# Optimization experiments

Hardware: AMD Instinct MI355X
Metric: run time of the kernel (lower is better)

Reference implementation:

```python
import jax, jax.numpy as jnp
import numpy as np

N = 50000   # nodes
E = 600000  # edges
D = 128     # in_feats = n_hidden
B = 16384   # pair batch
L = 2       # n_layers
C = 2       # n_classes
EPS = 1e-5


def setup_inputs() -> dict:
    key = jax.random.key(0)
    ks = jax.random.split(key, 16)
    s = 0.05
    return {
        "h": jax.random.normal(ks[0], (N, D), jnp.float32),
        "edge_src": jax.random.randint(ks[1], (E,), 0, N),
        "edge_dst": jax.random.randint(ks[2], (E,), 0, N),
        "x1": jax.random.randint(ks[3], (B,), 0, N),
        "x2": jax.random.randint(ks[4], (B,), 0, N),
        "x1_tar": jax.random.randint(ks[5], (B,), 0, N),
        "x2_tar": jax.random.randint(ks[6], (B,), 0, N),
        # SAGEConv params (mean aggregator): rst = h@W_self + mean_neigh@W_neigh + b
        "W_self": jax.random.normal(ks[7], (L, D, D), jnp.float32) * s,
        "W_neigh": jax.random.normal(ks[8], (L, D, D), jnp.float32) * s,
        "b_conv": jnp.zeros((L, D), jnp.float32),
        # head: linear1(3D->D) -> BN -> relu -> linear2(D->C)
        "W1": jax.random.normal(ks[9], (3 * D, D), jnp.float32) * s,
        "b1": jnp.zeros((D,), jnp.float32),
        "gamma": jnp.ones((D,), jnp.float32),
        "beta": jnp.zeros((D,), jnp.float32),
        "W2": jax.random.normal(ks[10], (D, C), jnp.float32) * s,
        "b2": jnp.zeros((C,), jnp.float32),
    }


def _sage_layers(h, edge_src, edge_dst, W_self, W_neigh, b_conv):
    # in-degree for mean aggregation (clamped to 1 to avoid div by 0)
    deg = jax.ops.segment_sum(jnp.ones((E,), h.dtype), edge_dst, num_segments=N)
    deg = jnp.maximum(deg, 1.0)[:, None]
    for l in range(L):
        msg = h[edge_src]                                        # [E, D] gather
        agg = jax.ops.segment_sum(msg, edge_dst, num_segments=N) / deg  # [N, D]
        h = jax.nn.relu(h @ W_self[l] + agg @ W_neigh[l] + b_conv[l])
    return h


def _pair_feat(h, a, b):
    ha, hb = h[a], h[b]
    return jnp.concatenate([ha, hb, jnp.abs(ha - hb)], axis=1)  # [B, 3D]


def _batchnorm(x, gamma, beta):
    m = x.mean(axis=0)
    v = x.var(axis=0)  # biased variance, as torch BN in training mode normalization
    return (x - m) * jax.lax.rsqrt(v + EPS) * gamma + beta


def reference(h, edge_src, edge_dst, x1, x2, x1_tar, x2_tar,
              W_self, W_neigh, b_conv, W1, b1, gamma, beta, W2, b2):
    h = _sage_layers(h, edge_src, edge_dst, W_self, W_neigh, b_conv)
    h_src = _pair_feat(h, x1, x2) @ W1 + b1
    h_tar = _pair_feat(h, x1_tar, x2_tar) @ W1 + b1
    h_src = _batchnorm(h_src, gamma, beta)
    h_tar = _batchnorm(h_tar, gamma, beta)
    h_src_mmd = jax.nn.relu(h_src)
    h_tar_mmd = jax.nn.relu(h_tar)
    h_p = h_src_mmd @ W2 + b2
    return (h_p, h_src_mmd, h_tar_mmd)
```

## Files before the change

kernel.cpp:

```cpp
#include <hip/hip_runtime.h>

#define NN 50000
#define NE 600000
#define DF 128
#define NB 16384
#define SCA_B 256
#define SCA_PER ((NE + SCA_B - 1) / SCA_B)
#define SCB_CAP 4352

typedef short bf16x8 __attribute__((ext_vector_type(8)));
typedef float f32x4 __attribute__((ext_vector_type(4)));

__device__ __forceinline__ float bf2f(unsigned short u){
  return __uint_as_float(((unsigned int)u) << 16);
}
__device__ __forceinline__ unsigned short f2bf(float x){
  unsigned int b = __float_as_uint(x);
  return (unsigned short)((b + 0x7FFFu + ((b >> 16) & 1u)) >> 16);
}

__global__ void GraphSAGE_8504035246140_kernel(){ }

__global__ __launch_bounds__(256) void k_prelude(
    const float* h_in, unsigned short* h_c,
    const float* Ws, const float* Wn, const float* W1,
    unsigned short* WsB, unsigned short* WnB, unsigned short* W1B,
    int* cnt, float* stats){
  int b = blockIdx.x, t = threadIdx.x;
  if (b < 3125){
    int i = b * 256 + t;
    const float4* s = (const float4*)h_in;
    float4 v0 = s[i * 2], v1 = s[i * 2 + 1];
    unsigned short d[8] = {f2bf(v0.x), f2bf(v0.y), f2bf(v0.z), f2bf(v0.w),
                           f2bf(v1.x), f2bf(v1.y), f2bf(v1.z), f2bf(v1.w)};
    *(bf16x8*)(h_c + i * 8) = *(bf16x8*)d;
  } else if (b < 3516){
    int i = (b - 3125) * 256 + t;
    if (i < 2 * NN) cnt[i] = 0;
  } else if (b < 3518){
    int i = (b - 3516) * 256 + t;
    if (i < 512) stats[i] = 0.f;
  } else {
    int idx = (b - 3518) * 256 + t;
    if (idx < 2 * DF * DF){
      int layer = idx >> 14;
      int e = idx & (DF * DF - 1);
      int k = e >> 7, n = e & 127;
      int dst = layer * DF * DF + (((k >> 3) * 128 + n) << 3) + (k & 7);
      WsB[dst] = f2bf(Ws[idx]);
      WnB[dst] = f2bf(Wn[idx]);
    }
    if (idx < 3 * DF * DF){
      int k = idx >> 7, n = idx & 127;
      W1B[(((k >> 3) * 128 + n) << 3) + (k & 7)] = f2bf(W1[idx]);
    }
  }
}

__global__ void k_hist(const int* dst, int* cnt){
  int e = blockIdx.x * 256 + threadIdx.x;
  if (e < NE) atomicAdd(&cnt[dst[e]], 1);
}
__global__ void k_scan1(const int* cnt, int* bsum){
  __shared__ int l[256];
  int t = threadIdx.x, i = blockIdx.x * 256 + t;
  l[t] = (i < NN) ? cnt[i] : 0;
  __syncthreads();
  for (int o = 128; o > 0; o >>= 1){
    if (t < o) l[t] += l[t + o];
    __syncthreads();
  }
  if (t == 0) bsum[blockIdx.x] = l[0];
}
__global__ void k_scan3(const int* cnt, const int* bsum, int* rp, int* cfill){
  __shared__ int bs[256];
  __shared__ int l[256];
  int t = threadIdx.x, i = blockIdx.x * 256 + t;
  bs[t] = (t < 196) ? bsum[t] : 0;
  int v = (i < NN) ? cnt[i] : 0;
  l[t] = v;
  __syncthreads();
  for (int o = 1; o < 256; o <<= 1){
    int xb = (t >= o) ? bs[t - o] : 0;
    int xl = (t >= o) ? l[t - o] : 0;
    __syncthreads();
    bs[t] += xb; l[t] += xl;
    __syncthreads();
  }
  int base = (blockIdx.x == 0) ? 0 : bs[blockIdx.x - 1];
  if (i < NN){
    int r = base + l[t] - v;
    rp[i] = r;
    if (t == 0) cfill[blockIdx.x] = r;
    if (i == NN - 1) rp[NN] = base + l[t];
  }
}

__global__ __launch_bounds__(256) void k_scatA(
    const int* src, const int* dst, int* cfill, unsigned int* tmp){
  __shared__ unsigned int hist[196];
  __shared__ unsigned int cursor[196];
  int t = threadIdx.x;
  int e0 = blockIdx.x * SCA_PER;
  int e1 = e0 + SCA_PER; if (e1 > NE) e1 = NE;
  if (t < 196) hist[t] = 0;
  __syncthreads();
  for (int e = e0 + t; e < e1; e += 256) atomicAdd(&hist[dst[e] >> 8], 1u);
  __syncthreads();
  if (t < 196) cursor[t] = (unsigned int)atomicAdd(&cfill[t], (int)hist[t]);
  __syncthreads();
  for (int e = e0 + t; e < e1; e += 256){
    int d = dst[e];
    unsigned int off = atomicAdd(&cursor[d >> 8], 1u);
    tmp[off] = (unsigned int)src[e] | ((unsigned int)(d & 255) << 16);
  }
}

__global__ __launch_bounds__(256) void k_scatB(
    const unsigned int* tmp, const int* rp, int* fill, int* perm){
  __shared__ unsigned int hist[256];
  __shared__ unsigned int sc[256];
  __shared__ unsigned int ebuf[SCB_CAP];
  __shared__ unsigned int sbuf[SCB_CAP];
  int b = blockIdx.x, t = threadIdx.x;
  int n0 = b << 8;
  int n1 = n0 + 256; if (n1 > NN) n1 = NN;
  int s = rp[n0], e = rp[n1];
  int cntb = e - s;
  if (cntb <= SCB_CAP){
    hist[t] = 0;
    __syncthreads();
    for (int i = t; i < cntb; i += 256){
      unsigned int v = tmp[s + i];
      ebuf[i] = v;
      atomicAdd(&hist[(v >> 16) & 255], 1u);
    }
    __syncthreads();
    unsigned int cntk = hist[t];
    sc[t] = cntk;
    __syncthreads();
    for (int o = 1; o < 256; o <<= 1){
      unsigned int x = (t >= o) ? sc[t - o] : 0;
      __syncthreads();
      sc[t] += x;
      __syncthreads();
    }
    hist[t] = sc[t] - cntk;
    __syncthreads();
    for (int i = t; i < cntb; i += 256){
      unsigned int v = ebuf[i];
      unsigned int off = atomicAdd(&hist[(v >> 16) & 255], 1u);
      sbuf[off] = v;
    }
    __syncthreads();
    for (int i = t; i < cntb; i += 256) perm[s + i] = (int)(sbuf[i] & 0xFFFFu);
  } else {
    for (int i = t; i < cntb; i += 256){
      unsigned int v = tmp[s + i];
      int node = n0 + (int)((v >> 16) & 255);
      int pos = atomicAdd(&fill[node], 1);
      perm[rp[node] + pos] = (int)(v & 0xFFFFu);
    }
  }
}

__global__ __launch_bounds__(256) void k_agg(
    const unsigned int* hb32, const int* rp, const int* perm,
    unsigned int* agg32){
  int n = blockIdx.x * 4 + (threadIdx.x >> 6);
  if (n >= NN) return;
  int l = threadIdx.x & 63;
  int rs = l >> 4, li = l & 15;
  int s = rp[n], e = rp[n + 1];
  const unsigned int* hq = hb32 + li * 4;
  float a0 = 0.f, a1 = 0.f, a2 = 0.f, a3 = 0.f;
  float a4 = 0.f, a5 = 0.f, a6 = 0.f, a7 = 0.f;
  int i = s;
  for (; i + 16 <= e; i += 16){
    int p0 = perm[i + rs];
    int p1 = perm[i + 4 + rs];
    int p2 = perm[i + 8 + rs];
    int p3 = perm[i + 12 + rs];
    uint4 x0 = *(const uint4*)(hq + (size_t)p0 * 64);
    uint4 x1 = *(const uint4*)(hq + (size_t)p1 * 64);
    uint4 x2 = *(const uint4*)(hq + (size_t)p2 * 64);
    uint4 x3 = *(const uint4*)(hq + (size_t)p3 * 64);
    a0 += __uint_as_float(x0.x << 16); a1 += __uint_as_float(x0.x & 0xffff0000u);
    a2 += __uint_as_float(x0.y << 16); a3 += __uint_as_float(x0.y & 0xffff0000u);
    a4 += __uint_as_float(x0.z << 16); a5 += __uint_as_float(x0.z & 0xffff0000u);
    a6 += __uint_as_float(x0.w << 16); a7 += __uint_as_float(x0.w & 0xffff0000u);
    a0 += __uint_as_float(x1.x << 16); a1 += __uint_as_float(x1.x & 0xffff0000u);
    a2 += __uint_as_float(x1.y << 16); a3 += __uint_as_float(x1.y & 0xffff0000u);
    a4 += __uint_as_float(x1.z << 16); a5 += __uint_as_float(x1.z & 0xffff0000u);
    a6 += __uint_as_float(x1.w << 16); a7 += __uint_as_float(x1.w & 0xffff0000u);
    a0 += __uint_as_float(x2.x << 16); a1 += __uint_as_float(x2.x & 0xffff0000u);
    a2 += __uint_as_float(x2.y << 16); a3 += __uint_as_float(x2.y & 0xffff0000u);
    a4 += __uint_as_float(x2.z << 16); a5 += __uint_as_float(x2.z & 0xffff0000u);
    a6 += __uint_as_float(x2.w << 16); a7 += __uint_as_float(x2.w & 0xffff0000u);
    a0 += __uint_as_float(x3.x << 16); a1 += __uint_as_float(x3.x & 0xffff0000u);
    a2 += __uint_as_float(x3.y << 16); a3 += __uint_as_float(x3.y & 0xffff0000u);
    a4 += __uint_as_float(x3.z << 16); a5 += __uint_as_float(x3.z & 0xffff0000u);
    a6 += __uint_as_float(x3.w << 16); a7 += __uint_as_float(x3.w & 0xffff0000u);
  }
  if (i < e){
    int i0 = i + rs, i1 = i + 4 + rs, i2 = i + 8 + rs, i3 = i + 12 + rs;
    int p0 = perm[i0 < e ? i0 : s];
    int p1 = perm[i1 < e ? i1 : s];
    int p2 = perm[i2 < e ? i2 : s];
    int p3 = perm[i3 < e ? i3 : s];
    uint4 x0 = *(const uint4*)(hq + (size_t)p0 * 64);
    uint4 x1 = *(const uint4*)(hq + (size_t)p1 * 64);
    uint4 x2 = *(const uint4*)(hq + (size_t)p2 * 64);
    uint4 x3 = *(const uint4*)(hq + (size_t)p3 * 64);
    if (i0 < e){
      a0 += __uint_as_float(x0.x << 16); a1 += __uint_as_float(x0.x & 0xffff0000u);
      a2 += __uint_as_float(x0.y << 16); a3 += __uint_as_float(x0.y & 0xffff0000u);
      a4 += __uint_as_float(x0.z << 16); a5 += __uint_as_float(x0.z & 0xffff0000u);
      a6 += __uint_as_float(x0.w << 16); a7 += __uint_as_float(x0.w & 0xffff0000u);
    }
    if (i1 < e){
      a0 += __uint_as_float(x1.x << 16); a1 += __uint_as_float(x1.x & 0xffff0000u);
      a2 += __uint_as_float(x1.y << 16); a3 += __uint_as_float(x1.y & 0xffff0000u);
      a4 += __uint_as_float(x1.z << 16); a5 += __uint_as_float(x1.z & 0xffff0000u);
      a6 += __uint_as_float(x1.w << 16); a7 += __uint_as_float(x1.w & 0xffff0000u);
    }
    if (i2 < e){
      a0 += __uint_as_float(x2.x << 16); a1 += __uint_as_float(x2.x & 0xffff0000u);
      a2 += __uint_as_float(x2.y << 16); a3 += __uint_as_float(x2.y & 0xffff0000u);
      a4 += __uint_as_float(x2.z << 16); a5 += __uint_as_float(x2.z & 0xffff0000u);
      a6 += __uint_as_float(x2.w << 16); a7 += __uint_as_float(x2.w & 0xffff0000u);
    }
    if (i3 < e){
      a0 += __uint_as_float(x3.x << 16); a1 += __uint_as_float(x3.x & 0xffff0000u);
      a2 += __uint_as_float(x3.y << 16); a3 += __uint_as_float(x3.y & 0xffff0000u);
      a4 += __uint_as_float(x3.z << 16); a5 += __uint_as_float(x3.z & 0xffff0000u);
      a6 += __uint_as_float(x3.w << 16); a7 += __uint_as_float(x3.w & 0xffff0000u);
    }
  }
  a0 += __shfl_xor(a0, 16); a1 += __shfl_xor(a1, 16);
  a2 += __shfl_xor(a2, 16); a3 += __shfl_xor(a3, 16);
  a4 += __shfl_xor(a4, 16); a5 += __shfl_xor(a5, 16);
  a6 += __shfl_xor(a6, 16); a7 += __shfl_xor(a7, 16);
  a0 += __shfl_xor(a0, 32); a1 += __shfl_xor(a1, 32);
  a2 += __shfl_xor(a2, 32); a3 += __shfl_xor(a3, 32);
  a4 += __shfl_xor(a4, 32); a5 += __shfl_xor(a5, 32);
  a6 += __shfl_xor(a6, 32); a7 += __shfl_xor(a7, 32);
  if (rs == 0){
    float di = 1.0f / fmaxf((float)(e - s), 1.0f);
    uint4 r;
    r.x = (unsigned int)f2bf(a0 * di) | ((unsigned int)f2bf(a1 * di) << 16);
    r.y = (unsigned int)f2bf(a2 * di) | ((unsigned int)f2bf(a3 * di) << 16);
    r.z = (unsigned int)f2bf(a4 * di) | ((unsigned int)f2bf(a5 * di) << 16);
    r.w = (unsigned int)f2bf(a6 * di) | ((unsigned int)f2bf(a7 * di) << 16);
    *(uint4*)(agg32 + (size_t)n * 64 + li * 4) = r;
  }
}

__global__ __launch_bounds__(256) void k_layer_mfma(
    const unsigned short* hb, const unsigned short* aggb,
    const unsigned short* WsB, const unsigned short* WnB,
    const float* bias, unsigned short* hout){
  int t = threadIdx.x;
  int w = t >> 6, l = t & 63;
  int m = l & 15, q = l >> 4;
  int r0 = blockIdx.x * 128 + w * 16;
  int arow0 = r0 + m;       if (arow0 > NN - 1) arow0 = NN - 1;
  int arow1 = r0 + 64 + m;  if (arow1 > NN - 1) arow1 = NN - 1;
  const unsigned short* hp0 = hb   + (size_t)arow0 * DF + q * 8;
  const unsigned short* ap0 = aggb + (size_t)arow0 * DF + q * 8;
  const unsigned short* hp1 = hb   + (size_t)arow1 * DF + q * 8;
  const unsigned short* ap1 = aggb + (size_t)arow1 * DF + q * 8;
  f32x4 acc0[8], acc1[8];
  for (int ct = 0; ct < 8; ++ct){
    float bbc = bias[ct * 16 + m];
    acc0[ct] = (f32x4){bbc, bbc, bbc, bbc};
    acc1[ct] = (f32x4){bbc, bbc, bbc, bbc};
  }
  for (int kt = 0; kt < 4; ++kt){
    bf16x8 a_h0 = *(const bf16x8*)(hp0 + kt * 32);
    bf16x8 a_g0 = *(const bf16x8*)(ap0 + kt * 32);
    bf16x8 a_h1 = *(const bf16x8*)(hp1 + kt * 32);
    bf16x8 a_g1 = *(const bf16x8*)(ap1 + kt * 32);
    int kg = kt * 4 + q;
    for (int ct = 0; ct < 8; ++ct){
      bf16x8 b_s = *(const bf16x8*)(WsB + (((kg << 7) + ct * 16 + m) << 3));
      bf16x8 b_n = *(const bf16x8*)(WnB + (((kg << 7) + ct * 16 + m) << 3));
      acc0[ct] = __builtin_amdgcn_mfma_f32_16x16x32_bf16(a_h0, b_s, acc0[ct], 0, 0, 0);
      acc0[ct] = __builtin_amdgcn_mfma_f32_16x16x32_bf16(a_g0, b_n, acc0[ct], 0, 0, 0);
      acc1[ct] = __builtin_amdgcn_mfma_f32_16x16x32_bf16(a_h1, b_s, acc1[ct], 0, 0, 0);
      acc1[ct] = __builtin_amdgcn_mfma_f32_16x16x32_bf16(a_g1, b_n, acc1[ct], 0, 0, 0);
    }
  }
  for (int ct = 0; ct < 8; ++ct){
    int col = ct * 16 + m;
    for (int reg = 0; reg < 4; ++reg){
      int row0 = r0 + q * 4 + reg;
      int row1 = row0 + 64;
      if (row0 < NN) hout[(size_t)row0 * DF + col] = f2bf(fmaxf(acc0[ct][reg], 0.f));
      if (row1 < NN) hout[(size_t)row1 * DF + col] = f2bf(fmaxf(acc1[ct][reg], 0.f));
    }
  }
}

__global__ __launch_bounds__(256) void k_pair_mfma(
    const unsigned short* h2,
    const int* x1, const int* x2, const int* x1t, const int* x2t,
    const unsigned short* W1B, const float* b1, float* zbase, float* stats){
  __shared__ __align__(16) unsigned short F[64 * 392];
  __shared__ float csum[128], csq[128];
  int g = blockIdx.y;
  const int* ia = g ? x1t : x1;
  const int* ib = g ? x2t : x2;
  float* z = zbase + (size_t)g * NB * DF;
  int t = threadIdx.x;
  if (t < 128){ csum[t] = 0.f; csq[t] = 0.f; }
  int r0 = blockIdx.x * 64;
  int i = t >> 2, qq = t & 3;
  int r = r0 + i;
  int a = ia[r], b = ib[r];
  const unsigned short* pa = h2 + (size_t)a * DF + qq * 32;
  const unsigned short* pb = h2 + (size_t)b * DF + qq * 32;
  unsigned short* fr = F + i * 392;
  for (int jj = 0; jj < 4; ++jj){
    bf16x8 va = *(const bf16x8*)(pa + jj * 8);
    bf16x8 vb = *(const bf16x8*)(pb + jj * 8);
    *(bf16x8*)(fr + qq * 32 + jj * 8) = va;
    *(bf16x8*)(fr + 128 + qq * 32 + jj * 8) = vb;
    unsigned short d[8];
    for (int e = 0; e < 8; ++e){
      float fa = bf2f((unsigned short)va[e]);
      float fb = bf2f((unsigned short)vb[e]);
      d[e] = f2bf(fabsf(fa - fb));
    }
    *(bf16x8*)(fr + 256 + qq * 32 + jj * 8) = *(bf16x8*)d;
  }
  __syncthreads();
  int w = t >> 6, l = t & 63;
  int m = l & 15, q = l >> 4;
  int rl = w * 16 + m;
  f32x4 acc[8];
  for (int ct = 0; ct < 8; ++ct){
    float bbc = b1[ct * 16 + m];
    acc[ct] = (f32x4){bbc, bbc, bbc, bbc};
  }
  for (int kt = 0; kt < 12; ++kt){
    bf16x8 af = *(const bf16x8*)(F + rl * 392 + kt * 32 + q * 8);
    int kg = kt * 4 + q;
    for (int ct = 0; ct < 8; ++ct){
      bf16x8 bfr = *(const bf16x8*)(W1B + (((kg << 7) + ct * 16 + m) << 3));
      acc[ct] = __builtin_amdgcn_mfma_f32_16x16x32_bf16(af, bfr, acc[ct], 0, 0, 0);
    }
  }
  for (int ct = 0; ct < 8; ++ct){
    int col = ct * 16 + m;
    int row = r0 + w * 16 + q * 4;
    float s = 0.f, s2 = 0.f;
    for (int reg = 0; reg < 4; ++reg){
      float v = acc[ct][reg];
      z[(size_t)(row + reg) * DF + col] = v;
      s += v; s2 += v * v;
    }
    atomicAdd(&csum[col], s);
    atomicAdd(&csq[col], s2);
  }
  __syncthreads();
  if (t < 128){
    atomicAdd(&stats[g * 256 + t], csum[t]);
    atomicAdd(&stats[g * 256 + 128 + t], csq[t]);
  }
}

__global__ __launch_bounds__(256) void k_norm_hp(
    const float* zbase, const float* stats,
    const float* gamma, const float* beta,
    const float* W2, const float* b2, float* mmd_base, float* hp){
  int g = blockIdx.y;
  int t = threadIdx.x;
  int w = t >> 6, l = t & 63;
  int c0 = l * 2, c1 = c0 + 1;
  float m0 = stats[g * 256 + c0] * (1.0f / NB);
  float m1 = stats[g * 256 + c1] * (1.0f / NB);
  float v0 = stats[g * 256 + 128 + c0] * (1.0f / NB) - m0 * m0;
  float v1 = stats[g * 256 + 128 + c1] * (1.0f / NB) - m1 * m1;
  float is0 = 1.0f / sqrtf(v0 + 1e-5f);
  float is1 = 1.0f / sqrtf(v1 + 1e-5f);
  float ga0 = gamma[c0], ga1 = gamma[c1];
  float be0 = beta[c0], be1 = beta[c1];
  float w200 = W2[c0 * 2], w201 = W2[c0 * 2 + 1];
  float w210 = W2[c1 * 2], w211 = W2[c1 * 2 + 1];
  const float* z = zbase + (size_t)g * NB * DF;
  float* mmd = mmd_base + (size_t)g * NB * DF;
  int rbase = blockIdx.x * 16 + w * 4;
  for (int rr = 0; rr < 4; ++rr){
    int row = rbase + rr;
    float2 zv = *(const float2*)(z + (size_t)row * DF + c0);
    float y0 = fmaxf((zv.x - m0) * is0 * ga0 + be0, 0.f);
    float y1 = fmaxf((zv.y - m1) * is1 * ga1 + be1, 0.f);
    float2 yv; yv.x = y0; yv.y = y1;
    *(float2*)(mmd + (size_t)row * DF + c0) = yv;
    if (g == 0){
      float s0 = y0 * w200 + y1 * w210;
      float s1 = y0 * w201 + y1 * w211;
      for (int o = 32; o > 0; o >>= 1){
        s0 += __shfl_xor(s0, o);
        s1 += __shfl_xor(s1, o);
      }
      if (l == 0){
        hp[row * 2]     = s0 + b2[0];
        hp[row * 2 + 1] = s1 + b2[1];
      }
    }
  }
}

extern "C" __attribute__((used, visibility("default")))
void kernel_launch(void* const* d_in, const int* in_sizes, int n_in,
                   void* d_out, int out_size, void* d_ws, size_t ws_size,
                   hipStream_t stream){
  const float* h_in  = (const float*)d_in[0];
  const int* esrc = (const int*)d_in[1];
  const int* edst = (const int*)d_in[2];
  const int* x1   = (const int*)d_in[3];
  const int* x2   = (const int*)d_in[4];
  const int* x1t  = (const int*)d_in[5];
  const int* x2t  = (const int*)d_in[6];
  const float* Wself = (const float*)d_in[7];
  const float* Wneigh= (const float*)d_in[8];
  const float* bconv = (const float*)d_in[9];
  const float* W1    = (const float*)d_in[10];
  const float* b1    = (const float*)d_in[11];
  const float* gamma = (const float*)d_in[12];
  const float* beta  = (const float*)d_in[13];
  const float* W2    = (const float*)d_in[14];
  const float* b2    = (const float*)d_in[15];
  float* out = (float*)d_out;
  float* hp_out   = out;
  float* mmd_base = out + 2 * NB;

  float* zreg  = (float*)d_ws;
  unsigned short* aggb = (unsigned short*)zreg;
  float* stats = zreg + (size_t)2 * NB * DF;
  float* mstd  = stats + 512;
  float* dinv  = mstd + 512;
  int* cnt  = (int*)(dinv + 50048);
  int* fill = cnt + NN;
  int* rp   = fill + NN;
  int* perm = rp + 50016;
  int* bsum = perm + 600000;
  int* cfill = bsum + 256;
  unsigned short* h_c = (unsigned short*)(cfill + 256);
  unsigned short* h1b = h_c + (size_t)NN * DF;
  unsigned short* h2b = h_c;
  unsigned short* WsB = h1b + (size_t)NN * DF;
  unsigned short* WnB = WsB + 2 * DF * DF;
  unsigned short* W1B = WnB + 2 * DF * DF;
  unsigned int* tmp = (unsigned int*)(W1B + 3 * DF * DF);
  (void)dinv;

  k_prelude<<<3710, 256, 0, stream>>>(h_in, h_c, Wself, Wneigh, W1,
                                      WsB, WnB, W1B, cnt, stats);

  k_hist<<<(NE + 255) / 256, 256, 0, stream>>>(edst, cnt);
  k_scan1<<<196, 256, 0, stream>>>(cnt, bsum);
  k_scan3<<<196, 256, 0, stream>>>(cnt, bsum, rp, cfill);
  k_scatA<<<SCA_B, 256, 0, stream>>>(esrc, edst, cfill, tmp);
  k_scatB<<<196, 256, 0, stream>>>(tmp, rp, fill, perm);

  k_agg<<<(NN + 3) / 4, 256, 0, stream>>>((const unsigned int*)h_c, rp, perm,
                                          (unsigned int*)aggb);
  k_layer_mfma<<<(NN + 127) / 128, 256, 0, stream>>>(h_c, aggb, WsB, WnB,
                                                     bconv, h1b);
  k_agg<<<(NN + 3) / 4, 256, 0, stream>>>((const unsigned int*)h1b, rp, perm,
                                          (unsigned int*)aggb);
  k_layer_mfma<<<(NN + 127) / 128, 256, 0, stream>>>(h1b, aggb, WsB + DF * DF,
                                                     WnB + DF * DF, bconv + DF,
                                                     h2b);

  k_pair_mfma<<<dim3(NB / 64, 2), 256, 0, stream>>>(h2b, x1, x2, x1t, x2t,
                                                    W1B, b1, zreg, stats);
  k_norm_hp<<<dim3(NB / 16, 2), 256, 0, stream>>>(zreg, stats, gamma, beta,
                                                  W2, b2, mmd_base, hp_out);
}
```

Baseline: 269.8 us.

## Build CSR from coarse bucket histogram, derive row pointers inside scatter pass

Replaces the per-node global-atomic histogram and two-kernel prefix scan with a shared-memory coarse histogram over 196 buckets of 256 nodes and a single-block scan. Per-node row pointers are now computed inside k_scatB from its local sort histogram, which removes the zeroing of the 100K-entry count and fill arrays. The overflow path now uses shared-memory cursors instead of global atomics. This cuts one kernel launch and most global atomic traffic, but adds a single-block kernel on the critical path.

```diff
diff --git a/kernel.cpp b/kernel.cpp
--- a/kernel.cpp
+++ b/kernel.cpp
@@ -6,6 +6,7 @@
 #define NB 16384
 #define SCA_B 256
 #define SCA_PER ((NE + SCA_B - 1) / SCA_B)
+#define NBKT 196
 #define SCB_CAP 4352
 
 typedef short bf16x8 __attribute__((ext_vector_type(8)));
@@ -25,7 +26,7 @@
     const float* h_in, unsigned short* h_c,
     const float* Ws, const float* Wn, const float* W1,
     unsigned short* WsB, unsigned short* WnB, unsigned short* W1B,
-    int* cnt, float* stats){
+    int* chist, float* stats){
   int b = blockIdx.x, t = threadIdx.x;
   if (b < 3125){
     int i = b * 256 + t;
@@ -34,14 +35,13 @@
     unsigned short d[8] = {f2bf(v0.x), f2bf(v0.y), f2bf(v0.z), f2bf(v0.w),
                            f2bf(v1.x), f2bf(v1.y), f2bf(v1.z), f2bf(v1.w)};
     *(bf16x8*)(h_c + i * 8) = *(bf16x8*)d;
-  } else if (b < 3516){
+  } else if (b < 3127){
     int i = (b - 3125) * 256 + t;
-    if (i < 2 * NN) cnt[i] = 0;
-  } else if (b < 3518){
-    int i = (b - 3516) * 256 + t;
     if (i < 512) stats[i] = 0.f;
+  } else if (b < 3128){
+    if (t < NBKT) chist[t] = 0;
   } else {
-    int idx = (b - 3518) * 256 + t;
+    int idx = (b - 3128) * 256 + t;
     if (idx < 2 * DF * DF){
       int layer = idx >> 14;
       int e = idx & (DF * DF - 1);
@@ -57,57 +57,51 @@
   }
 }
 
-__global__ void k_hist(const int* dst, int* cnt){
-  int e = blockIdx.x * 256 + threadIdx.x;
-  if (e < NE) atomicAdd(&cnt[dst[e]], 1);
-}
-__global__ void k_scan1(const int* cnt, int* bsum){
-  __shared__ int l[256];
-  int t = threadIdx.x, i = blockIdx.x * 256 + t;
-  l[t] = (i < NN) ? cnt[i] : 0;
-  __syncthreads();
-  for (int o = 128; o > 0; o >>= 1){
-    if (t < o) l[t] += l[t + o];
+__global__ __launch_bounds__(256) void k_chist(const int* dst, int* chist){
+  __shared__ int h[NBKT];
+  int t = threadIdx.x;
+  if (t < NBKT) h[t] = 0;
+  __syncthreads();
+  int e0 = blockIdx.x * SCA_PER;
+  int e1 = e0 + SCA_PER; if (e1 > NE) e1 = NE;
+  for (int e = e0 + t; e < e1; e += 256) atomicAdd(&h[dst[e] >> 8], 1);
+  __syncthreads();
+  if (t < NBKT && h[t]) atomicAdd(&chist[t], h[t]);
+}
+
+__global__ __launch_bounds__(256) void k_cscan(
+    const int* chist, int* cfill, int* bbase){
+  __shared__ int sc[256];
+  int t = threadIdx.x;
+  int v = (t < NBKT) ? chist[t] : 0;
+  sc[t] = v;
+  __syncthreads();
+  for (int o = 1; o < 256; o <<= 1){
+    int x = (t >= o) ? sc[t - o] : 0;
     __syncthreads();
-  }
-  if (t == 0) bsum[blockIdx.x] = l[0];
-}
-__global__ void k_scan3(const int* cnt, const int* bsum, int* rp, int* cfill){
-  __shared__ int bs[256];
-  __shared__ int l[256];
-  int t = threadIdx.x, i = blockIdx.x * 256 + t;
-  bs[t] = (t < 196) ? bsum[t] : 0;
-  int v = (i < NN) ? cnt[i] : 0;
-  l[t] = v;
-  __syncthreads();
-  for (int o = 1; o < 256; o <<= 1){
-    int xb = (t >= o) ? bs[t - o] : 0;
-    int xl = (t >= o) ? l[t - o] : 0;
+    sc[t] += x;
     __syncthreads();
-    bs[t] += xb; l[t] += xl;
-    __syncthreads();
-  }
-  int base = (blockIdx.x == 0) ? 0 : bs[blockIdx.x - 1];
-  if (i < NN){
-    int r = base + l[t] - v;
-    rp[i] = r;
-    if (t == 0) cfill[blockIdx.x] = r;
-    if (i == NN - 1) rp[NN] = base + l[t];
-  }
+  }
+  if (t < NBKT){
+    int base = sc[t] - v;
+    cfill[t] = base;
+    bbase[t] = base;
+  }
+  if (t == 0) bbase[NBKT] = NE;
 }
 
 __global__ __launch_bounds__(256) void k_scatA(
     const int* src, const int* dst, int* cfill, unsigned int* tmp){
-  __shared__ unsigned int hist[196];
-  __shared__ unsigned int cursor[196];
+  __shared__ unsigned int hist[NBKT];
+  __shared__ unsigned int cursor[NBKT];
   int t = threadIdx.x;
   int e0 = blockIdx.x * SCA_PER;
   int e1 = e0 + SCA_PER; if (e1 > NE) e1 = NE;
-  if (t < 196) hist[t] = 0;
+  if (t < NBKT) hist[t] = 0;
   __syncthreads();
   for (int e = e0 + t; e < e1; e += 256) atomicAdd(&hist[dst[e] >> 8], 1u);
   __syncthreads();
-  if (t < 196) cursor[t] = (unsigned int)atomicAdd(&cfill[t], (int)hist[t]);
+  if (t < NBKT) cursor[t] = (unsigned int)atomicAdd(&cfill[t], (int)hist[t]);
   __syncthreads();
   for (int e = e0 + t; e < e1; e += 256){
     int d = dst[e];
@@ -117,36 +111,45 @@
 }
 
 __global__ __launch_bounds__(256) void k_scatB(
-    const unsigned int* tmp, const int* rp, int* fill, int* perm){
+    const unsigned int* tmp, const int* bbase, int* rp, int* perm){
   __shared__ unsigned int hist[256];
   __shared__ unsigned int sc[256];
   __shared__ unsigned int ebuf[SCB_CAP];
   __shared__ unsigned int sbuf[SCB_CAP];
   int b = blockIdx.x, t = threadIdx.x;
   int n0 = b << 8;
-  int n1 = n0 + 256; if (n1 > NN) n1 = NN;
-  int s = rp[n0], e = rp[n1];
+  int s = bbase[b], e = bbase[b + 1];
   int cntb = e - s;
-  if (cntb <= SCB_CAP){
-    hist[t] = 0;
-    __syncthreads();
+  bool fits = (cntb <= SCB_CAP);
+  hist[t] = 0;
+  __syncthreads();
+  if (fits){
     for (int i = t; i < cntb; i += 256){
       unsigned int v = tmp[s + i];
       ebuf[i] = v;
       atomicAdd(&hist[(v >> 16) & 255], 1u);
     }
+  } else {
+    for (int i = t; i < cntb; i += 256)
+      atomicAdd(&hist[(tmp[s + i] >> 16) & 255], 1u);
+  }
+  __syncthreads();
+  unsigned int cntk = hist[t];
+  sc[t] = cntk;
+  __syncthreads();
+  for (int o = 1; o < 256; o <<= 1){
+    unsigned int x = (t >= o) ? sc[t - o] : 0;
     __syncthreads();
-    unsigned int cntk = hist[t];
-    sc[t] = cntk;
+    sc[t] += x;
     __syncthreads();
-    for (int o = 1; o < 256; o <<= 1){
-      unsigned int x = (t >= o) ? sc[t - o] : 0;
-      __syncthreads();
-      sc[t] += x;
-      __syncthreads();
-    }
-    hist[t] = sc[t] - cntk;
-    __syncthreads();
+  }
+  unsigned int excl = sc[t] - cntk;
+  int node = n0 + t;
+  if (node < NN) rp[node] = s + (int)excl;
+  if (b == NBKT - 1 && t == 0) rp[NN] = NE;
+  hist[t] = excl;
+  __syncthreads();
+  if (fits){
     for (int i = t; i < cntb; i += 256){
       unsigned int v = ebuf[i];
       unsigned int off = atomicAdd(&hist[(v >> 16) & 255], 1u);
@@ -157,9 +160,8 @@
   } else {
     for (int i = t; i < cntb; i += 256){
       unsigned int v = tmp[s + i];
-      int node = n0 + (int)((v >> 16) & 255);
-      int pos = atomicAdd(&fill[node], 1);
-      perm[rp[node] + pos] = (int)(v & 0xFFFFu);
+      unsigned int off = atomicAdd(&hist[(v >> 16) & 255], 1u);
+      perm[s + (int)off] = (int)(v & 0xFFFFu);
     }
   }
 }
@@ -442,9 +444,9 @@
   float* stats = zreg + (size_t)2 * NB * DF;
   float* mstd  = stats + 512;
   float* dinv  = mstd + 512;
-  int* cnt  = (int*)(dinv + 50048);
-  int* fill = cnt + NN;
-  int* rp   = fill + NN;
+  int* bbase = (int*)(dinv + 50048);
+  int* chist = bbase + 256;
+  int* rp   = chist + 256;
   int* perm = rp + 50016;
   int* bsum = perm + 600000;
   int* cfill = bsum + 256;
@@ -455,16 +457,15 @@
   unsigned short* WnB = WsB + 2 * DF * DF;
   unsigned short* W1B = WnB + 2 * DF * DF;
   unsigned int* tmp = (unsigned int*)(W1B + 3 * DF * DF);
-  (void)dinv;
-
-  k_prelude<<<3710, 256, 0, stream>>>(h_in, h_c, Wself, Wneigh, W1,
-                                      WsB, WnB, W1B, cnt, stats);
-
-  k_hist<<<(NE + 255) / 256, 256, 0, stream>>>(edst, cnt);
-  k_scan1<<<196, 256, 0, stream>>>(cnt, bsum);
-  k_scan3<<<196, 256, 0, stream>>>(cnt, bsum, rp, cfill);
+  (void)dinv; (void)bsum;
+
+  k_prelude<<<3320, 256, 0, stream>>>(h_in, h_c, Wself, Wneigh, W1,
+                                      WsB, WnB, W1B, chist, stats);
+
+  k_chist<<<SCA_B, 256, 0, stream>>>(edst, chist);
+  k_cscan<<<1, 256, 0, stream>>>(chist, cfill, bbase);
   k_scatA<<<SCA_B, 256, 0, stream>>>(esrc, edst, cfill, tmp);
-  k_scatB<<<196, 256, 0, stream>>>(tmp, rp, fill, perm);
+  k_scatB<<<NBKT, 256, 0, stream>>>(tmp, bbase, rp, perm);
 
   k_agg<<<(NN + 3) / 4, 256, 0, stream>>>((const unsigned int*)h_c, rp, perm,
                                           (unsigned int*)aggb);
```

Result: faster. 243.8 us, median of 2 (-9.6%).
